# Kernel tuning notes

Hardware: AMD Instinct MI355X
Metric: run time of the kernel (lower is better)

The kernel has to match this reference:

```python
import jax, jax.numpy as jnp
import numpy as np

B, S, D, H = 2, 2048, 1024, 16
DH = D // H
DFF = 4 * D
EPS = 1e-5
NEG = -1e9


def _layernorm(x, gamma, beta):
    mu = jnp.mean(x, axis=-1, keepdims=True)
    var = jnp.mean(jnp.square(x - mu), axis=-1, keepdims=True)
    return (x - mu) * jax.lax.rsqrt(var + EPS) * gamma + beta


def setup_inputs() -> dict:
    key = jax.random.key(0)
    ks = jax.random.split(key, 12)
    s = 0.02
    X = jax.random.normal(ks[0], (B, S, D), dtype=jnp.float32)
    # causal mask (True = attend)
    attention_mask = jnp.tril(jnp.ones((S, S), dtype=bool))
    return {
        "X": X,
        "attention_mask": attention_mask,
        "gamma1": jnp.ones((D,), jnp.float32),
        "beta1": jnp.zeros((D,), jnp.float32),
        "Wq": jax.random.normal(ks[1], (H, D, DH), jnp.float32) * s,
        "bq": jnp.zeros((H, DH), jnp.float32),
        "Wk": jax.random.normal(ks[2], (H, D, DH), jnp.float32) * s,
        "bk": jnp.zeros((H, DH), jnp.float32),
        "Wv": jax.random.normal(ks[3], (H, D, DH), jnp.float32) * s,
        "bv": jnp.zeros((H, DH), jnp.float32),
        "W0": jax.random.normal(ks[4], (D, D), jnp.float32) * s,
        "b0": jnp.zeros((D,), jnp.float32),
        "gamma2": jnp.ones((D,), jnp.float32),
        "beta2": jnp.zeros((D,), jnp.float32),
        "W1": jax.random.normal(ks[5], (D, DFF), jnp.float32) * s,
        "b1": jnp.zeros((DFF,), jnp.float32),
        "W2": jax.random.normal(ks[6], (DFF, D), jnp.float32) * s,
        "b2": jnp.zeros((D,), jnp.float32),
    }


def reference(X, attention_mask, gamma1, beta1, Wq, bq, Wk, bk, Wv, bv, W0, b0,
              gamma2, beta2, W1, b1, W2, b2):
    scale = 1.0 / np.sqrt(DH)
    # --- pre-LN MHA ---
    Xn = _layernorm(X, gamma1, beta1)
    # per-head projections, stacked: [B,H,S,DH]
    Q = jnp.einsum('bsd,hdk->bhsk', Xn, Wq) + bq[None, :, None, :]
    K = jnp.einsum('bsd,hdk->bhsk', Xn, Wk) + bk[None, :, None, :]
    V = jnp.einsum('bsd,hdk->bhsk', Xn, Wv) + bv[None, :, None, :]
    scores = jnp.einsum('bhsk,bhtk->bhst', Q, K) * scale
    scores = jnp.where(attention_mask, scores, NEG)
    weights = jax.nn.softmax(scores, axis=-1)
    attn = jnp.einsum('bhst,bhtv->bhsv', weights, V)  # [B,H,S,DH]
    # concat heads (head-major along feature dim, matching torch.cat order)
    attn = attn.transpose(0, 2, 1, 3).reshape(B, S, D)
    mha = attn @ W0 + b0
    X = mha + X  # residual (dropout = identity at eval)
    # --- pre-LN FFN ---
    Xn2 = _layernorm(X, gamma2, beta2)
    h = jax.nn.relu(Xn2 @ W1 + b1)
    ffn = h @ W2 + b2
    return ffn + X
```

## Files before the change

kernel.cpp:

```cpp
#include <hip/hip_runtime.h>
#include <hip/hip_bf16.h>

#define BB 2
#define SS 2048
#define DDIM 1024
#define HH 16
#define DHH 64
#define DFF_ 4096
#define BS 4096
#define NQKV 3072

typedef unsigned short u16;
using short8  = __attribute__((ext_vector_type(8))) short;
using floatx4 = __attribute__((ext_vector_type(4))) float;
using ushort4_t = __attribute__((ext_vector_type(4))) unsigned short;

__device__ __forceinline__ u16 f2b(float f){
  union { unsigned int u; float f; } v; v.f = f;
  unsigned int u = v.u;
  u += 0x7FFFu + ((u >> 16) & 1u);
  return (u16)(u >> 16);
}

__device__ __forceinline__ void gl2lds16(const u16* g, u16* l){
  __builtin_amdgcn_global_load_lds((const __attribute__((address_space(1))) void*)g,
                                   (__attribute__((address_space(3))) void*)l, 16, 0, 0);
}

__device__ __forceinline__ void ln_row(const float* __restrict__ x,
                                       const float* __restrict__ gamma,
                                       const float* __restrict__ beta,
                                       u16* __restrict__ y, int row, float* smem){
  const float4* xr = (const float4*)(x + (size_t)row * DDIM);
  int tid = threadIdx.x;
  float4 v = xr[tid];
  float s  = v.x + v.y + v.z + v.w;
  float ss = v.x*v.x + v.y*v.y + v.z*v.z + v.w*v.w;
  for (int o = 1; o < 64; o <<= 1){ s += __shfl_xor(s, o, 64); ss += __shfl_xor(ss, o, 64); }
  int wid = tid >> 6;
  if ((tid & 63) == 0){ smem[wid] = s; smem[wid + 4] = ss; }
  __syncthreads();
  s  = smem[0] + smem[1] + smem[2] + smem[3];
  ss = smem[4] + smem[5] + smem[6] + smem[7];
  float mu  = s / (float)DDIM;
  float var = ss / (float)DDIM - mu * mu;
  float rs  = rsqrtf(var + 1e-5f);
  const float4* gp = (const float4*)gamma;
  const float4* bp = (const float4*)beta;
  float4 g = gp[tid], b = bp[tid];
  u16* yr = y + (size_t)row * DDIM + tid*4;
  yr[0] = f2b((v.x - mu) * rs * g.x + b.x);
  yr[1] = f2b((v.y - mu) * rs * g.y + b.y);
  yr[2] = f2b((v.z - mu) * rs * g.z + b.z);
  yr[3] = f2b((v.w - mu) * rs * g.w + b.w);
}

__device__ __forceinline__ void tcast(const float* __restrict__ in, u16* __restrict__ out,
                                      int R, int C, int tile, float (*sh)[33]){
  int nr = R >> 5;
  int tr = tile % nr, tc = tile / nr;
  int r0 = tr * 32, c0 = tc * 32;
  int tx = threadIdx.x & 31, ty = threadIdx.x >> 5;
  for (int i = ty; i < 32; i += 8)
    sh[i][tx] = in[(size_t)(r0 + i) * C + c0 + tx];
  __syncthreads();
  for (int i = ty; i < 32; i += 8)
    out[(size_t)(c0 + i) * R + r0 + tx] = f2b(sh[tx][i]);
}

__global__ __launch_bounds__(256) void prep_ln1_k(
    const float* __restrict__ X, const float* __restrict__ g1, const float* __restrict__ be1,
    u16* __restrict__ Xn,
    const float* __restrict__ Wq, const float* __restrict__ Wk, const float* __restrict__ Wv,
    const float* __restrict__ W0, const float* __restrict__ W1,
    const float* __restrict__ bq, const float* __restrict__ bk, const float* __restrict__ bv,
    u16* __restrict__ wqkvT, u16* __restrict__ w0T, u16* __restrict__ w1T,
    float* __restrict__ biasQKV)
{
  __shared__ float sh[32][33];
  __shared__ float smem8[8];
  int id = blockIdx.x;
  if (id < 4096){
    ln_row(X, g1, be1, Xn, id, smem8);
  } else if (id < 7168){
    int lid2 = id - 4096;
    int which = lid2 >> 10, lid = lid2 & 1023;
    const float* src = which == 0 ? Wq : (which == 1 ? Wk : Wv);
    u16* dst = wqkvT + (size_t)which * 1048576;
    int bat = lid >> 6, t = lid & 63;
    tcast(src + (size_t)bat * 65536, dst + (size_t)bat * 65536, 1024, 64, t, sh);
  } else if (id < 8192){
    tcast(W0, w0T, 1024, 1024, id - 7168, sh);
  } else if (id < 12288){
    tcast(W1, w1T, 1024, 4096, id - 8192, sh);
  } else {
    int idx = (id - 12288) * 256 + threadIdx.x;
    if (idx < 3072){
      float v = idx < 1024 ? bq[idx] : (idx < 2048 ? bk[idx - 1024] : bv[idx - 2048]);
      biasQKV[idx] = v;
    }
  }
}

__global__ __launch_bounds__(256) void w2t_ln2_k(
    const float* __restrict__ X1, const float* __restrict__ g2, const float* __restrict__ be2,
    u16* __restrict__ Xn2, const float* __restrict__ W2, u16* __restrict__ w2T)
{
  __shared__ float sh[32][33];
  __shared__ float smem8[8];
  int id = blockIdx.x;
  if (id < 4096){
    ln_row(X1, g2, be2, Xn2, id, smem8);
  } else {
    int tile = id - 4096;
    int tr = tile / 32, tc = tile % 32;
    int r0 = tr * 32, c0 = tc * 32;
    int tx = threadIdx.x & 31, ty = threadIdx.x >> 5;
    for (int i = ty; i < 32; i += 8)
      sh[i][tx] = W2[(size_t)(r0 + i) * 1024 + c0 + tx];
    __syncthreads();
    for (int i = ty; i < 32; i += 8)
      w2T[(size_t)(c0 + i) * 4096 + r0 + tx] = f2b(sh[tx][i]);
  }
}

__global__ __launch_bounds__(256) void vt_k(const u16* __restrict__ QKV, u16* __restrict__ VT){
  __shared__ u16 t[32][33];
  int bh = blockIdx.z; int b = bh >> 4, h = bh & 15;
  int s0 = blockIdx.x * 32, d0 = blockIdx.y * 32;
  int tx = threadIdx.x & 31, ty = threadIdx.x >> 5;
  const u16* src = QKV + (size_t)b * SS * NQKV + 2048 + h * DHH;
  for (int i = ty; i < 32; i += 8)
    t[i][tx] = src[(size_t)(s0 + i) * NQKV + d0 + tx];
  __syncthreads();
  u16* dst = VT + (size_t)bh * DHH * SS;
  for (int i = ty; i < 32; i += 8)
    dst[(size_t)(d0 + i) * SS + s0 + tx] = t[tx][i];
}

template<int TM, int TN>
__global__ __launch_bounds__(256) void gemm_db(
    const u16* __restrict__ A, const u16* __restrict__ Bt,
    const float* __restrict__ bias, const float* __restrict__ res,
    void* __restrict__ Cv, int M, int N, int K, int relu, int writeBf16)
{
  constexpr int ACH = TM / 16;
  constexpr int BCH = TN / 16;
  constexpr int CH1 = ACH + BCH;
  constexpr int CPW = (2 * CH1) / 4;
  constexpr int MI  = TM / 32;
  constexpr int NI  = TN / 32;

  __shared__ __align__(16) u16 As[2][2][TM * 32];
  __shared__ __align__(16) u16 Bs[2][2][TN * 32];

  int tid  = threadIdx.x;
  int wave = tid >> 6, lane = tid & 63;
  int quad = lane >> 4, l16 = lane & 15;

  int gx = gridDim.x, gy = gridDim.y;
  int bid = blockIdx.x + gx * blockIdx.y;
  int xcd = bid & 7, idx = bid >> 3;
  int by  = xcd * (gy >> 3) + idx / gx;
  int bx  = idx % gx;

  int m0 = by * TM, n0 = bx * TN;
  int wm = (wave >> 1) * (TM / 2), wn = (wave & 1) * (TN / 2);

  floatx4 acc[MI][NI] = {};

  int srow = lane >> 2;
  int scol = (lane & 3) * 8;
  const u16* gptr[CPW]; u16* lp0[CPW]; int lstep[CPW];
#pragma unroll
  for (int k = 0; k < CPW; k++){
    int c = wave * CPW + k;
    int p = c / CH1, cc = c % CH1;
    if (cc < ACH){
      gptr[k]  = A + (size_t)(m0 + cc*16 + srow) * K + p*32 + scol;
      lp0[k]   = &As[0][p][cc * 512];
      lstep[k] = 2 * TM * 32;
    } else {
      gptr[k]  = Bt + (size_t)(n0 + (cc-ACH)*16 + srow) * K + p*32 + scol;
      lp0[k]   = &Bs[0][p][(cc-ACH) * 512];
      lstep[k] = 2 * TN * 32;
    }
  }

  int nsteps = K >> 6;

#pragma unroll
  for (int k = 0; k < CPW; k++){ gl2lds16(gptr[k], lp0[k]); gptr[k] += 64; }
  asm volatile("s_waitcnt vmcnt(0)" ::: "memory");
  __builtin_amdgcn_sched_barrier(0);
  __builtin_amdgcn_s_barrier();
  __builtin_amdgcn_sched_barrier(0);

  for (int t = 0; t < nsteps; ++t){
    int cur = t & 1;
    if (t + 1 < nsteps){
#pragma unroll
      for (int k = 0; k < CPW; k++){
        gl2lds16(gptr[k], lp0[k] + (cur ? 0 : lstep[k]));
        gptr[k] += 64;
      }
    }
    __builtin_amdgcn_s_setprio(1);
#pragma unroll
    for (int p = 0; p < 2; p++){
      short8 af[MI], bf[NI];
#pragma unroll
      for (int i = 0; i < MI; i++)
        af[i] = *(short8*)&As[cur][p][(wm + i*16 + l16)*32 + quad*8];
#pragma unroll
      for (int j = 0; j < NI; j++)
        bf[j] = *(short8*)&Bs[cur][p][(wn + j*16 + l16)*32 + quad*8];
#pragma unroll
      for (int i = 0; i < MI; i++)
#pragma unroll
        for (int j = 0; j < NI; j++)
          acc[i][j] = __builtin_amdgcn_mfma_f32_16x16x32_bf16(bf[j], af[i], acc[i][j], 0,0,0);
    }
    __builtin_amdgcn_s_setprio(0);
    if (t + 1 < nsteps){
      asm volatile("s_waitcnt vmcnt(0)" ::: "memory");
      __builtin_amdgcn_sched_barrier(0);
      __builtin_amdgcn_s_barrier();
      __builtin_amdgcn_sched_barrier(0);
    }
  }

  u16*   Cb = (u16*)Cv;
  float* Cf = (float*)Cv;
#pragma unroll
  for (int i = 0; i < MI; i++){
    int row = m0 + wm + i*16 + l16;
#pragma unroll
    for (int j = 0; j < NI; j++){
      int col = n0 + wn + j*16 + quad*4;
      float v0 = acc[i][j][0], v1 = acc[i][j][1], v2 = acc[i][j][2], v3 = acc[i][j][3];
      if (bias){
        const float4 bb = *(const float4*)&bias[col];
        v0 += bb.x; v1 += bb.y; v2 += bb.z; v3 += bb.w;
      }
      if (relu){
        v0 = v0 > 0.f ? v0 : 0.f; v1 = v1 > 0.f ? v1 : 0.f;
        v2 = v2 > 0.f ? v2 : 0.f; v3 = v3 > 0.f ? v3 : 0.f;
      }
      if (res){
        const float4 rr = *(const float4*)&res[(size_t)row * N + col];
        v0 += rr.x; v1 += rr.y; v2 += rr.z; v3 += rr.w;
      }
      if (writeBf16){
        ushort4_t o = { f2b(v0), f2b(v1), f2b(v2), f2b(v3) };
        *(ushort4_t*)&Cb[(size_t)row * N + col] = o;
      } else {
        float4 o; o.x = v0; o.y = v1; o.z = v2; o.w = v3;
        *(float4*)&Cf[(size_t)row * N + col] = o;
      }
    }
  }
}

#define KT 128

__global__ __launch_bounds__(512) void attn_k(
    const u16* __restrict__ QKV, const u16* __restrict__ VT, u16* __restrict__ O)
{
  int bh = blockIdx.x;
  int b = bh >> 4, h = bh & 15;
  int t  = (int)gridDim.y - 1 - blockIdx.y;
  const u16* Qb_  = QKV + (size_t)b * SS * NQKV + h * DHH;
  const u16* Kb_  = Qb_ + 1024;
  const u16* VTb_ = VT + (size_t)bh * DHH * SS;

  __shared__ __align__(16) u16 Ks [KT * 64];
  __shared__ __align__(16) u16 VTs[DHH * 128];
  __shared__ __align__(16) u16 Ps [8][16 * 128];

  int tid = threadIdx.x;
  int wave = tid >> 6, lane = tid & 63;
  int g = wave >> 2, w = wave & 3;
  int quad = lane >> 4, l16 = lane & 15;
  int qrow = t * 128 + g * 64 + w * 16;

  short8 qf0, qf1;
  {
    const u16* qp = Qb_ + (size_t)(qrow + l16) * NQKV + quad*8;
    qf0 = *(const short8*)qp;
    qf1 = *(const short8*)(qp + 32);
  }

  float lsum = 0.f;
  floatx4 oacc[4] = {};

  int nk = t + 1;
  int lim = w + 4 * g;
  int qcol = qrow + l16;
  const float qs = 0.125f * 1.44269504088896f;

  short8 kreg[2], vreg[2];
#pragma unroll
  for (int it = 0; it < 2; it++){
    int gg = tid + it * 512;
    kreg[it] = *(const short8*)(Kb_ + (size_t)(gg >> 3) * NQKV + (gg & 7) * 8);
    vreg[it] = *(const short8*)(VTb_ + (size_t)(gg >> 4) * SS + (gg & 15) * 8);
  }

  for (int kt = 0; kt < nk; kt++){
    int k0 = kt * KT;
    __syncthreads();
#pragma unroll
    for (int it = 0; it < 2; it++){
      int gg = tid + it * 512;
      { int row = gg >> 3, idx = (row * 64 + (gg & 7) * 8) ^ ((row & 7) << 3);
        *(short8*)&Ks[idx] = kreg[it]; }
      { int row = gg >> 4, idx = (row * 128 + (gg & 15) * 8) ^ ((row & 7) << 3);
        *(short8*)&VTs[idx] = vreg[it]; }
    }
    __syncthreads();

    if (kt + 1 < nk){
      int kn = k0 + KT;
#pragma unroll
      for (int it = 0; it < 2; it++){
        int gg = tid + it * 512;
        kreg[it] = *(const short8*)(Kb_ + (size_t)(kn + (gg >> 3)) * NQKV + (gg & 7) * 8);
        vreg[it] = *(const short8*)(VTb_ + (size_t)(gg >> 4) * SS + kn + (gg & 15) * 8);
      }
    }

    bool last = (kt == nk - 1);
    int stmax = last ? lim : 7;
    floatx4 sacc[8] = {};
    __builtin_amdgcn_s_setprio(1);
#pragma unroll
    for (int st = 0; st < 8; st++){
      if (st <= stmax){
        int r0i = (st*16 + l16) * 64;
        int sw  = (l16 & 7) << 3;
        short8 kb0 = *(short8*)&Ks[(r0i + quad*8) ^ sw];
        short8 kb1 = *(short8*)&Ks[(r0i + 32 + quad*8) ^ sw];
        sacc[st] = __builtin_amdgcn_mfma_f32_16x16x32_bf16(kb0, qf0, sacc[st], 0,0,0);
        sacc[st] = __builtin_amdgcn_mfma_f32_16x16x32_bf16(kb1, qf1, sacc[st], 0,0,0);
      }
    }
    __builtin_amdgcn_s_setprio(0);

#pragma unroll
    for (int st = 0; st < 8; st++){
      int base = (l16 * 128 + st*16 + quad*4) ^ ((l16 & 7) << 3);
      if (st <= stmax){
        float e0 = exp2f(sacc[st][0] * qs);
        float e1 = exp2f(sacc[st][1] * qs);
        float e2 = exp2f(sacc[st][2] * qs);
        float e3 = exp2f(sacc[st][3] * qs);
        if (last){
          int colb = k0 + st*16 + quad*4;
          e0 = (colb + 0 <= qcol) ? e0 : 0.f;
          e1 = (colb + 1 <= qcol) ? e1 : 0.f;
          e2 = (colb + 2 <= qcol) ? e2 : 0.f;
          e3 = (colb + 3 <= qcol) ? e3 : 0.f;
        }
        lsum += (e0 + e1) + (e2 + e3);
        unsigned int lo, hi;
        asm("v_cvt_pk_bf16_f32 %0, %1, %2" : "=v"(lo) : "v"(e0), "v"(e1));
        asm("v_cvt_pk_bf16_f32 %0, %1, %2" : "=v"(hi) : "v"(e2), "v"(e3));
        uint2 pk; pk.x = lo; pk.y = hi;
        *(uint2*)&Ps[wave][base] = pk;
      } else {
        uint2 z; z.x = 0u; z.y = 0u;
        *(uint2*)&Ps[wave][base] = z;
      }
    }
    asm volatile("s_waitcnt lgkmcnt(0)" ::: "memory");

    int cmax = last ? (lim >> 1) : 3;
    short8 pa[4];
#pragma unroll
    for (int c = 0; c < 4; c++)
      pa[c] = *(short8*)&Ps[wave][(l16 * 128 + c*32 + quad*8) ^ ((l16 & 7) << 3)];
    __builtin_amdgcn_s_setprio(1);
#pragma unroll
    for (int ost = 0; ost < 4; ost++){
#pragma unroll
      for (int c = 0; c < 4; c++){
        if (c <= cmax){
          short8 vb = *(short8*)&VTs[((ost*16 + l16) * 128 + c*32 + quad*8) ^ ((l16 & 7) << 3)];
          oacc[ost] = __builtin_amdgcn_mfma_f32_16x16x32_bf16(pa[c], vb, oacc[ost], 0,0,0);
        }
      }
    }
    __builtin_amdgcn_s_setprio(0);
  }

  lsum += __shfl_xor(lsum, 16, 64);
  lsum += __shfl_xor(lsum, 32, 64);
  float linv = 1.0f / lsum;
  float inv[4];
#pragma unroll
  for (int r = 0; r < 4; r++)
    inv[r] = __shfl(linv, quad*4 + r, 64);

#pragma unroll
  for (int ost = 0; ost < 4; ost++)
#pragma unroll
    for (int r = 0; r < 4; r++){
      int s  = qrow + quad*4 + r;
      int dh = ost*16 + l16;
      O[((size_t)b * SS + s) * DDIM + h * DHH + dh] = f2b(oacc[ost][r] * inv[r]);
    }
}

extern "C" void kernel_launch(void* const* d_in, const int* in_sizes, int n_in,
                              void* d_out, int out_size, void* d_ws, size_t ws_size,
                              hipStream_t stream) {
  const float* X   = (const float*)d_in[0];
  const float* g1  = (const float*)d_in[2];
  const float* be1 = (const float*)d_in[3];
  const float* Wq  = (const float*)d_in[4];
  const float* bq  = (const float*)d_in[5];
  const float* Wk  = (const float*)d_in[6];
  const float* bk  = (const float*)d_in[7];
  const float* Wv  = (const float*)d_in[8];
  const float* bv  = (const float*)d_in[9];
  const float* W0  = (const float*)d_in[10];
  const float* b0  = (const float*)d_in[11];
  const float* g2  = (const float*)d_in[12];
  const float* be2 = (const float*)d_in[13];
  const float* W1  = (const float*)d_in[14];
  const float* b1  = (const float*)d_in[15];
  const float* W2  = (const float*)d_in[16];
  const float* b2  = (const float*)d_in[17];
  float* out = (float*)d_out;

  u16* ws16 = (u16*)d_ws;
  u16* wqkvT = ws16;
  u16* w0T   = ws16 + 3145728;
  u16* w2T   = ws16;
  u16* w1T   = ws16 + 4194304;
  u16* QKVb  = ws16 + 8388608;
  u16* VTb   = ws16 + 8388608 + 12582912;
  u16* hb    = ws16 + 8388608;
  u16* Xn    = ws16 + 25165824;
  u16* attnB = Xn;
  float* biasQKV = (float*)(ws16 + 29360128);

  prep_ln1_k<<<dim3(12300), 256, 0, stream>>>(X, g1, be1, Xn,
      Wq, Wk, Wv, W0, W1, bq, bk, bv, wqkvT, w0T, w1T, biasQKV);

  gemm_db<128,128><<<dim3(24, 32), 256, 0, stream>>>(Xn, wqkvT, biasQKV, nullptr, QKVb,
      BS, NQKV, 1024, 0, 1);

  vt_k<<<dim3(64, 2, 32), 256, 0, stream>>>(QKVb, VTb);

  attn_k<<<dim3(32, 16), 512, 0, stream>>>(QKVb, VTb, attnB);

  gemm_db<64,128><<<dim3(8, 64), 256, 0, stream>>>(attnB, w0T, b0, X, out,
      BS, DDIM, 1024, 0, 0);

  w2t_ln2_k<<<dim3(8192), 256, 0, stream>>>(out, g2, be2, Xn, W2, w2T);

  gemm_db<128,128><<<dim3(32, 32), 256, 0, stream>>>(Xn, w1T, b1, nullptr, hb,
      BS, DFF_, 1024, 1, 1);
  gemm_db<64,128><<<dim3(8, 64), 256, 0, stream>>>(hb, w2T, b2, out, out,
      BS, DDIM, DFF_, 0, 0);
}
```

Measured before the change: 368.8 us.

## Deepen GEMM LDS pipeline to four-stage ring with partial vmcnt waits

Replaces the double-buffered K=64 LDS staging in the bf16 GEMM with a four-slot ring of K=32 stages, prefetching three stages ahead. Partial vmcnt waits replace the full drain, so global-to-LDS loads overlap several MFMA steps. It keeps the same LDS footprint but halves the work per barrier, doubling the barrier count, and correctness depends on the hardcoded vmcnt immediates for CPW of 3 or 4.

```diff
diff --git a/kernel.cpp b/kernel.cpp
--- a/kernel.cpp
+++ b/kernel.cpp
@@ -14,6 +14,8 @@
 using short8  = __attribute__((ext_vector_type(8))) short;
 using floatx4 = __attribute__((ext_vector_type(4))) float;
 using ushort4_t = __attribute__((ext_vector_type(4))) unsigned short;
+
+#define VMW(n) asm volatile("s_waitcnt vmcnt(" #n ")" ::: "memory")
 
 __device__ __forceinline__ u16 f2b(float f){
   union { unsigned int u; float f; } v; v.f = f;
@@ -147,12 +149,13 @@
   constexpr int ACH = TM / 16;
   constexpr int BCH = TN / 16;
   constexpr int CH1 = ACH + BCH;
-  constexpr int CPW = (2 * CH1) / 4;
+  constexpr int CPW = CH1 / 4;
   constexpr int MI  = TM / 32;
   constexpr int NI  = TN / 32;
-
-  __shared__ __align__(16) u16 As[2][2][TM * 32];
-  __shared__ __align__(16) u16 Bs[2][2][TN * 32];
+  static_assert(CPW == 3 || CPW == 4, "vmcnt immediates assume CPW in {3,4}");
+
+  __shared__ __align__(16) u16 As[4][TM * 32];
+  __shared__ __align__(16) u16 Bs[4][TN * 32];
 
   int tid  = threadIdx.x;
   int wave = tid >> 6, lane = tid & 63;
@@ -171,59 +174,70 @@
 
   int srow = lane >> 2;
   int scol = (lane & 3) * 8;
-  const u16* gptr[CPW]; u16* lp0[CPW]; int lstep[CPW];
+  const u16* gptr[CPW]; u16* lp0[CPW]; int bstep[CPW];
 #pragma unroll
   for (int k = 0; k < CPW; k++){
     int c = wave * CPW + k;
-    int p = c / CH1, cc = c % CH1;
-    if (cc < ACH){
-      gptr[k]  = A + (size_t)(m0 + cc*16 + srow) * K + p*32 + scol;
-      lp0[k]   = &As[0][p][cc * 512];
-      lstep[k] = 2 * TM * 32;
+    if (c < ACH){
+      gptr[k]  = A + (size_t)(m0 + c*16 + srow) * K + scol;
+      lp0[k]   = &As[0][c * 512];
+      bstep[k] = TM * 32;
     } else {
-      gptr[k]  = Bt + (size_t)(n0 + (cc-ACH)*16 + srow) * K + p*32 + scol;
-      lp0[k]   = &Bs[0][p][(cc-ACH) * 512];
-      lstep[k] = 2 * TN * 32;
-    }
-  }
-
-  int nsteps = K >> 6;
-
-#pragma unroll
-  for (int k = 0; k < CPW; k++){ gl2lds16(gptr[k], lp0[k]); gptr[k] += 64; }
-  asm volatile("s_waitcnt vmcnt(0)" ::: "memory");
+      int cb = c - ACH;
+      gptr[k]  = Bt + (size_t)(n0 + cb*16 + srow) * K + scol;
+      lp0[k]   = &Bs[0][cb * 512];
+      bstep[k] = TN * 32;
+    }
+  }
+
+  int nsteps = K >> 5;
+
+#pragma unroll
+  for (int pt = 0; pt < 3; pt++){
+#pragma unroll
+    for (int k = 0; k < CPW; k++){
+      gl2lds16(gptr[k], lp0[k] + pt * bstep[k]);
+      gptr[k] += 32;
+    }
+  }
+  if constexpr (CPW == 4) VMW(8); else VMW(6);
   __builtin_amdgcn_sched_barrier(0);
   __builtin_amdgcn_s_barrier();
   __builtin_amdgcn_sched_barrier(0);
 
   for (int t = 0; t < nsteps; ++t){
-    int cur = t & 1;
+    if (t + 3 < nsteps){
+      int bi = (t + 3) & 3;
+#pragma unroll
+      for (int k = 0; k < CPW; k++){
+        gl2lds16(gptr[k], lp0[k] + bi * bstep[k]);
+        gptr[k] += 32;
+      }
+    }
+    int cur = t & 3;
+    __builtin_amdgcn_s_setprio(1);
+    short8 af[MI], bf[NI];
+#pragma unroll
+    for (int i = 0; i < MI; i++)
+      af[i] = *(short8*)&As[cur][(wm + i*16 + l16)*32 + quad*8];
+#pragma unroll
+    for (int j = 0; j < NI; j++)
+      bf[j] = *(short8*)&Bs[cur][(wn + j*16 + l16)*32 + quad*8];
+#pragma unroll
+    for (int i = 0; i < MI; i++)
+#pragma unroll
+      for (int j = 0; j < NI; j++)
+        acc[i][j] = __builtin_amdgcn_mfma_f32_16x16x32_bf16(bf[j], af[i], acc[i][j], 0,0,0);
+    __builtin_amdgcn_s_setprio(0);
+
     if (t + 1 < nsteps){
-#pragma unroll
-      for (int k = 0; k < CPW; k++){
-        gl2lds16(gptr[k], lp0[k] + (cur ? 0 : lstep[k]));
-        gptr[k] += 64;
-      }
-    }
-    __builtin_amdgcn_s_setprio(1);
-#pragma unroll
-    for (int p = 0; p < 2; p++){
-      short8 af[MI], bf[NI];
-#pragma unroll
-      for (int i = 0; i < MI; i++)
-        af[i] = *(short8*)&As[cur][p][(wm + i*16 + l16)*32 + quad*8];
-#pragma unroll
-      for (int j = 0; j < NI; j++)
-        bf[j] = *(short8*)&Bs[cur][p][(wn + j*16 + l16)*32 + quad*8];
-#pragma unroll
-      for (int i = 0; i < MI; i++)
-#pragma unroll
-        for (int j = 0; j < NI; j++)
-          acc[i][j] = __builtin_amdgcn_mfma_f32_16x16x32_bf16(bf[j], af[i], acc[i][j], 0,0,0);
-    }
-    __builtin_amdgcn_s_setprio(0);
-    if (t + 1 < nsteps){
-      asm volatile("s_waitcnt vmcnt(0)" ::: "memory");
+      if (t < nsteps - 3){
+        if constexpr (CPW == 4) VMW(8); else VMW(6);
+      } else if (t == nsteps - 3){
+        if constexpr (CPW == 4) VMW(4); else VMW(3);
+      } else {
+        VMW(0);
+      }
       __builtin_amdgcn_sched_barrier(0);
       __builtin_amdgcn_s_barrier();
       __builtin_amdgcn_sched_barrier(0);
```

Result: slower. 396.5 us (+7.5%).
